# Performance work log

Measured on AMD Instinct MI355X. Metric: run time of the kernel, lower is better.

Reference implementation:

```python
import jax, jax.numpy as jnp
import numpy as np

DIM = 768
H = 12
HD = 64  # head_dim = dim // num_heads
SCALE = HD ** (-0.5)
EPS = 1e-6


def setup_inputs() -> dict:
    key = jax.random.key(0)
    k1, k2, k3, k4, k5 = jax.random.split(key, 5)
    B, N = 8, 1024
    x = jax.random.normal(k1, (B, N, DIM), dtype=jnp.float32)
    policy = jax.random.uniform(k2, (B, N, 1), dtype=jnp.float32)
    # nn.Linear weights: [out_features, in_features]; qkv_bias=False, proj has bias
    qkv_w = jax.random.normal(k3, (3 * H * HD, DIM), dtype=jnp.float32) * (DIM ** -0.5)
    proj_w = jax.random.normal(k4, (DIM, H * HD), dtype=jnp.float32) * ((H * HD) ** -0.5)
    proj_b = jax.random.normal(k5, (DIM,), dtype=jnp.float32) * 0.01
    return {"x": x, "policy": policy, "qkv_w": qkv_w, "proj_w": proj_w, "proj_b": proj_b}


def _softmax_with_policy(attn, policy):
    # attn: [B,H,N,N], policy: [B,N,1]
    B, Hh, N, _ = attn.shape
    attn_policy = policy.reshape(B, 1, 1, N)
    eye = jnp.eye(N, dtype=attn_policy.dtype).reshape(1, 1, N, N)
    attn_policy = attn_policy + (1.0 - attn_policy) * eye
    max_att = jnp.max(attn, axis=-1, keepdims=True)
    a = jnp.exp((attn - max_att).astype(jnp.float32)) * attn_policy.astype(jnp.float32)
    a = (a + EPS / N) / (jnp.sum(a, axis=-1, keepdims=True) + EPS)
    return a.astype(max_att.dtype)


def reference(x, policy, qkv_w, proj_w, proj_b):
    B, N, C = x.shape
    qkv = (x @ qkv_w.T).reshape(B, N, 3, H, HD)
    qkv = jnp.transpose(qkv, (2, 0, 3, 1, 4))  # [3,B,H,N,HD]
    q, k, v = qkv[0], qkv[1], qkv[2]
    attn = jnp.einsum('bhnd,bhmd->bhnm', q * SCALE, k)  # [B,H,N,N]
    attn = _softmax_with_policy(attn, policy)
    out = jnp.einsum('bhnm,bhmd->bhnd', attn, v)  # [B,H,N,HD]
    out = jnp.transpose(out, (0, 2, 1, 3)).reshape(B, N, H * HD)
    return out @ proj_w.T + proj_b
```

## Files before the change

### kernel.cpp

```cpp
#include <hip/hip_runtime.h>

typedef __bf16 bf16x8 __attribute__((ext_vector_type(8)));
typedef float floatx4 __attribute__((ext_vector_type(4)));

#define EPSF 1e-6f

__device__ inline unsigned short f2bf(float f) {
  union { float f; unsigned u; } x; x.f = f;
  unsigned r = x.u + 0x7FFFu + ((x.u >> 16) & 1u);
  return (unsigned short)(r >> 16);
}
__device__ inline float bf2f(unsigned short u) {
  union { unsigned u; float f; } x; x.u = ((unsigned)u) << 16;
  return x.f;
}
__device__ inline unsigned pk2bf(float lo, float hi) {
  union { float f; unsigned u; } a, b; a.f = lo; b.f = hi;
  unsigned ua = a.u + 0x8000u, ub = b.u + 0x8000u;
  return (ub & 0xFFFF0000u) | (ua >> 16);
}
__device__ inline float fexp2(float x) { return __builtin_amdgcn_exp2f(x); }

__device__ inline floatx4 mfma16(bf16x8 a, bf16x8 b, floatx4 c) {
  return __builtin_amdgcn_mfma_f32_16x16x32_bf16(a, b, c, 0, 0, 0);
}

__device__ inline void gll16(const unsigned short* g, unsigned short* l) {
  __builtin_amdgcn_global_load_lds((__attribute__((address_space(1))) void*)g,
                                   (__attribute__((address_space(3))) void*)l, 16, 0, 0);
}

__device__ __host__ inline int sigma_inv(int p) {
  const int qq = p >> 3, jj = p & 7;
  return (jj < 4) ? (qq * 4 + jj) : (16 + qq * 4 + jj - 4);
}

__global__ __launch_bounds__(256) void prep_kernel(const float* __restrict__ x,
                                                   const float* __restrict__ qkv_w,
                                                   const float* __restrict__ proj_w,
                                                   const float* __restrict__ policy,
                                                   unsigned short* __restrict__ xb,
                                                   unsigned short* __restrict__ wqkv,
                                                   unsigned short* __restrict__ wproj,
                                                   unsigned short* __restrict__ pbf) {
  const int bid = blockIdx.x, tid = threadIdx.x;
  if (bid < 3072) {
    const int i = bid * 2048 + tid * 8;
    float4 v0 = *(const float4*)(x + i);
    float4 v1 = *(const float4*)(x + i + 4);
    __align__(16) unsigned short o[8] = {f2bf(v0.x), f2bf(v0.y), f2bf(v0.z), f2bf(v0.w),
                                         f2bf(v1.x), f2bf(v1.y), f2bf(v1.z), f2bf(v1.w)};
    *(float4*)(xb + i) = *(float4*)o;
  } else if (bid < 3936) {
    const int i = (bid - 3072) * 2048 + tid * 8;
    const float s = (i < 589824) ? 0.18033688011112042f : 1.0f;
    float4 v0 = *(const float4*)(qkv_w + i);
    float4 v1 = *(const float4*)(qkv_w + i + 4);
    __align__(16) unsigned short o[8] = {
        f2bf(v0.x * s), f2bf(v0.y * s), f2bf(v0.z * s), f2bf(v0.w * s),
        f2bf(v1.x * s), f2bf(v1.y * s), f2bf(v1.z * s), f2bf(v1.w * s)};
    *(float4*)(wqkv + i) = *(float4*)o;
  } else if (bid < 4224) {
    const int i0 = (bid - 3936) * 2048 + tid * 8;
    const int base = (i0 / 768) * 768 + ((i0 % 768) & ~63);
    __align__(16) unsigned short o[8];
#pragma unroll
    for (int t = 0; t < 8; t++) {
      const int cp = (i0 + t) & 63;
      const int c = 16 * (cp & 3) + (cp >> 2);
      o[t] = f2bf(proj_w[base + c]);
    }
    *(float4*)(wproj + i0) = *(float4*)o;
  } else {
    const int idx = (bid - 4224) * 256 + tid;
    const int b = idx >> 10, g = idx & 1023;
    const int c = ((g >> 5) << 5) + sigma_inv(g & 31);
    pbf[idx] = f2bf(policy[b * 1024 + c]);
  }
}

template <int EP, int BN>
__global__ __launch_bounds__(256, 3) void gemm_bt(const unsigned short* __restrict__ A,
                                                  const unsigned short* __restrict__ Bt,
                                                  void* __restrict__ Cout,
                                                  const float* __restrict__ bias,
                                                  int M, int N, int K) {
  constexpr int J = BN / 32;
  __shared__ __align__(16) unsigned short sA[128 * 64];
  __shared__ __align__(16) unsigned short sB[BN * 64];
  const int m0 = blockIdx.y * 128, n0 = blockIdx.x * BN;
  const int tid = threadIdx.x;
  const int lane = tid & 63, wave = tid >> 6;
  const int qd = lane >> 4, l15 = lane & 15;
  const int wr = (wave >> 1) * 64, wc = (wave & 1) * (BN / 2);
  const int srow = tid >> 3;
  const int scb = (tid & 7) ^ (srow & 7);
  const unsigned short* Ag = A + (long)(m0 + srow) * K + scb * 8;
  const unsigned short* Bg = Bt + (long)(n0 + srow) * K + scb * 8;
  const int x7 = l15 & 7;
  floatx4 acc[4][J] = {};
  for (int k0 = 0; k0 < K; k0 += 64) {
    __syncthreads();
#pragma unroll
    for (int p = 0; p < 4; p++) gll16(Ag + (long)(p * 32) * K + k0, sA + p * 2048 + wave * 512);
#pragma unroll
    for (int p = 0; p < J; p++) gll16(Bg + (long)(p * 32) * K + k0, sB + p * 2048 + wave * 512);
    __syncthreads();
#pragma unroll
    for (int s = 0; s < 2; s++) {
      const int cw = ((s * 4 + qd) ^ x7) * 8;
      bf16x8 af[4], bf[J];
#pragma unroll
      for (int i = 0; i < 4; i++) af[i] = *(const bf16x8*)&sA[(wr + i * 16 + l15) * 64 + cw];
#pragma unroll
      for (int j = 0; j < J; j++) bf[j] = *(const bf16x8*)&sB[(wc + j * 16 + l15) * 64 + cw];
#pragma unroll
      for (int i = 0; i < 4; i++)
#pragma unroll
        for (int j = 0; j < J; j++) acc[i][j] = mfma16(af[i], bf[j], acc[i][j]);
    }
  }
  if constexpr (EP == 0) {
#pragma unroll
    for (int i = 0; i < 4; i++)
#pragma unroll
      for (int r = 0; r < 4; r++) {
        const int row = m0 + wr + i * 16 + qd * 4 + r;
        __align__(8) unsigned short pk[4];
#pragma unroll
        for (int j = 0; j < 4; j++) pk[j] = f2bf(acc[i][j][r]);
        *(uint2*)((unsigned short*)Cout + (long)row * N + n0 + wc + 4 * l15) = *(uint2*)pk;
      }
  } else {
#pragma unroll
    for (int i = 0; i < 4; i++)
#pragma unroll
      for (int j = 0; j < J; j++) {
        const int col = n0 + wc + j * 16 + l15;
#pragma unroll
        for (int r = 0; r < 4; r++) {
          const int row = m0 + wr + i * 16 + qd * 4 + r;
          ((float*)Cout)[(long)row * N + col] = acc[i][j][r] + bias[col];
        }
      }
  }
}

__global__ __launch_bounds__(256) void transpose_v(const unsigned short* __restrict__ qkv,
                                                   const float* __restrict__ policy,
                                                   unsigned short* __restrict__ vTp) {
  __shared__ unsigned short tile[64][72];
  __shared__ float sPol[64];
  const int bh = blockIdx.y;
  const int b = bh / 12, h = bh % 12;
  const int n0 = blockIdx.x * 64;
  const int t = threadIdx.x;
  if (t < 64) sPol[t] = policy[b * 1024 + n0 + t];
  {
    const int nr = t >> 2, dc = (t & 3) * 16;
    const unsigned short* src = qkv + (long)(b * 1024 + n0 + nr) * 2304 + 2 * 768 + h * 64 + dc;
    float4 v0 = *(const float4*)src;
    float4 v1 = *(const float4*)(src + 8);
    *(float4*)&tile[nr][dc] = v0;
    *(float4*)&tile[nr][dc + 8] = v1;
  }
  __syncthreads();
  {
    const int d = t >> 2, nc = (t & 3) * 16;
    __align__(16) unsigned short o[16];
#pragma unroll
    for (int jj = 0; jj < 16; jj++) {
      const int cc = nc + jj;
      const int cl = (cc & 32) + sigma_inv(cc & 31);
      o[jj] = f2bf(bf2f(tile[cl][d]) * sPol[cl]);
    }
    unsigned short* dst = vTp + (long)(bh * 64 + d) * 1024 + n0 + nc;
    *(float4*)dst = *(float4*)&o[0];
    *(float4*)(dst + 8) = *(float4*)&o[8];
  }
}

__global__ __launch_bounds__(256, 3) void attn_kernel(const unsigned short* __restrict__ qkv,
                                                      const unsigned short* __restrict__ vTp,
                                                      const unsigned short* __restrict__ pbf,
                                                      const float* __restrict__ policy,
                                                      unsigned short* __restrict__ aout) {
  __shared__ __align__(16) unsigned short sK[2][2048];
  __shared__ __align__(16) unsigned short sV[2][2048];
  __shared__ __align__(16) unsigned short sPv[1024];
  __shared__ float sD[4][32];
  const int bid = blockIdx.x;
  const int bh = bid % 96, qt = bid / 96;
  const int b = bh / 12, h = bh % 12;
  const int tid = threadIdx.x;
  const int wave = tid >> 6, lane = tid & 63;
  const int qd = lane >> 4, l15 = lane & 15;
  const int q0 = qt * 128 + wave * 32;
  const unsigned short* qb = qkv + (long)(b * 1024 + q0 + l15) * 2304 + h * 64 + qd * 8;
  bf16x8 qf00 = *(const bf16x8*)qb;
  bf16x8 qf01 = *(const bf16x8*)(qb + 32);
  bf16x8 qf10 = *(const bf16x8*)(qb + (long)16 * 2304);
  bf16x8 qf11 = *(const bf16x8*)(qb + (long)16 * 2304 + 32);
  if (tid < 128) *(float4*)(sPv + tid * 8) = *(const float4*)(pbf + b * 1024 + tid * 8);
  const int krow = wave * 8 + (lane >> 3);
  const int kcb = (lane & 7) ^ (lane >> 3);
  const unsigned short* kgl = qkv + (long)(b * 1024 + krow) * 2304 + 768 + h * 64 + kcb * 8;
  const int vrow = tid >> 2;
  const int vcb = (tid & 3) ^ ((vrow ^ (vrow >> 2)) & 3);
  const unsigned short* vgl = vTp + (long)(bh * 64 + vrow) * 1024 + vcb * 8;
  const int x7 = l15 & 7;
  const int vsw = (qd ^ ((l15 ^ (l15 >> 2)) & 3)) * 8;
  floatx4 O0[4] = {}, O1[4] = {};
  floatx4 Dl0 = {}, Dl1 = {};
  gll16(kgl, &sK[0][wave * 512]);
  gll16(vgl, &sV[0][wave * 512]);
  __builtin_amdgcn_s_waitcnt(0);
  __syncthreads();
  for (int it = 0; it < 32; ++it) {
    const int buf = it & 1;
    if (it < 31) {
      gll16(kgl + (long)(32 * (it + 1)) * 2304, &sK[buf ^ 1][wave * 512]);
      gll16(vgl + 32 * (it + 1), &sV[buf ^ 1][wave * 512]);
    }
    const int c0 = it * 32;
    bf16x8 k00 = *(const bf16x8*)&sK[buf][(0 * 16 + l15) * 64 + ((0 + qd) ^ x7) * 8];
    bf16x8 k01 = *(const bf16x8*)&sK[buf][(0 * 16 + l15) * 64 + ((4 + qd) ^ x7) * 8];
    bf16x8 k10 = *(const bf16x8*)&sK[buf][(1 * 16 + l15) * 64 + ((0 + qd) ^ x7) * 8];
    bf16x8 k11 = *(const bf16x8*)&sK[buf][(1 * 16 + l15) * 64 + ((4 + qd) ^ x7) * 8];
    bf16x8 pv = *(const bf16x8*)&sPv[c0 + qd * 8];
    floatx4 z = {0.f, 0.f, 0.f, 0.f};
    floatx4 tA0 = mfma16(k01, qf01, mfma16(k00, qf00, z));
    floatx4 tB0 = mfma16(k11, qf01, mfma16(k10, qf00, z));
    floatx4 tA1 = mfma16(k01, qf11, mfma16(k00, qf10, z));
    floatx4 tB1 = mfma16(k11, qf11, mfma16(k10, qf10, z));
    uint4 pu0, pu1;
    pu0.x = pk2bf(fexp2(tA0[0]), fexp2(tA0[1]));
    pu0.y = pk2bf(fexp2(tA0[2]), fexp2(tA0[3]));
    pu0.z = pk2bf(fexp2(tB0[0]), fexp2(tB0[1]));
    pu0.w = pk2bf(fexp2(tB0[2]), fexp2(tB0[3]));
    pu1.x = pk2bf(fexp2(tA1[0]), fexp2(tA1[1]));
    pu1.y = pk2bf(fexp2(tA1[2]), fexp2(tA1[3]));
    pu1.z = pk2bf(fexp2(tB1[0]), fexp2(tB1[1]));
    pu1.w = pk2bf(fexp2(tB1[2]), fexp2(tB1[3]));
    bf16x8 pf0 = *(bf16x8*)&pu0;
    bf16x8 pf1 = *(bf16x8*)&pu1;
    bf16x8 vf0 = *(const bf16x8*)&sV[buf][(0 * 16 + l15) * 32 + vsw];
    bf16x8 vf1 = *(const bf16x8*)&sV[buf][(1 * 16 + l15) * 32 + vsw];
    bf16x8 vf2 = *(const bf16x8*)&sV[buf][(2 * 16 + l15) * 32 + vsw];
    bf16x8 vf3 = *(const bf16x8*)&sV[buf][(3 * 16 + l15) * 32 + vsw];
    Dl0 = mfma16(pf0, pv, Dl0);
    Dl1 = mfma16(pf1, pv, Dl1);
    O0[0] = mfma16(pf0, vf0, O0[0]); O1[0] = mfma16(pf1, vf0, O1[0]);
    O0[1] = mfma16(pf0, vf1, O0[1]); O1[1] = mfma16(pf1, vf1, O1[1]);
    O0[2] = mfma16(pf0, vf2, O0[2]); O1[2] = mfma16(pf1, vf2, O1[2]);
    O0[3] = mfma16(pf0, vf3, O0[3]); O1[3] = mfma16(pf1, vf3, O1[3]);
    __builtin_amdgcn_s_waitcnt(0);
    __syncthreads();
  }
  {
    const unsigned short* kd = qkv + (long)(b * 1024 + q0 + l15) * 2304 + 768 + h * 64 + qd * 8;
    bf16x8 kd00 = *(const bf16x8*)kd;
    bf16x8 kd01 = *(const bf16x8*)(kd + 32);
    bf16x8 kd10 = *(const bf16x8*)(kd + (long)16 * 2304);
    bf16x8 kd11 = *(const bf16x8*)(kd + (long)16 * 2304 + 32);
    float part0 = 0.f, part1 = 0.f;
#pragma unroll
    for (int jj = 0; jj < 8; jj++) {
      part0 += (float)qf00[jj] * (float)kd00[jj] + (float)qf01[jj] * (float)kd01[jj];
      part1 += (float)qf10[jj] * (float)kd10[jj] + (float)qf11[jj] * (float)kd11[jj];
    }
    part0 += __shfl_xor(part0, 16); part0 += __shfl_xor(part0, 32);
    part1 += __shfl_xor(part1, 16); part1 += __shfl_xor(part1, 32);
    const float p0 = policy[b * 1024 + q0 + l15];
    const float p1 = policy[b * 1024 + q0 + 16 + l15];
    if (qd == 0) {
      sD[wave][l15] = fexp2(part0) * (1.0f - p0);
      sD[wave][16 + l15] = fexp2(part1) * (1.0f - p1);
    }
    __builtin_amdgcn_s_waitcnt(0);
    const unsigned short* vdiag = qkv + (long)(b * 1024 + q0) * 2304 + 1536 + h * 64 + l15;
#pragma unroll
    for (int r = 0; r < 4; r++) {
      const int row = qd * 4 + r;
      const float c0v = sD[wave][row], c1v = sD[wave][16 + row];
#pragma unroll
      for (int j = 0; j < 4; j++) {
        O0[j][r] += c0v * bf2f(vdiag[(long)row * 2304 + j * 16]);
        O1[j][r] += c1v * bf2f(vdiag[(long)(16 + row) * 2304 + j * 16]);
      }
      Dl0[r] += c0v;
      Dl1[r] += c1v;
    }
  }
  const long ob = (long)(b * 1024 + q0 + qd * 4) * 768 + h * 64 + l15;
#pragma unroll
  for (int r = 0; r < 4; r++) {
    const float li0 = 1.0f / (Dl0[r] + EPSF);
    const float li1 = 1.0f / (Dl1[r] + EPSF);
#pragma unroll
    for (int j = 0; j < 4; j++) {
      aout[ob + (long)r * 768 + j * 16] = f2bf(O0[j][r] * li0);
      aout[ob + (long)(16 * 768) + r * 768 + j * 16] = f2bf(O1[j][r] * li1);
    }
  }
}

extern "C" void kernel_launch(void* const* d_in, const int* in_sizes, int n_in,
                              void* d_out, int out_size, void* d_ws, size_t ws_size,
                              hipStream_t stream) {
  const float* x      = (const float*)d_in[0];
  const float* policy = (const float*)d_in[1];
  const float* qkv_w  = (const float*)d_in[2];
  const float* proj_w = (const float*)d_in[3];
  const float* proj_b = (const float*)d_in[4];
  float* out = (float*)d_out;

  char* ws = (char*)d_ws;
  unsigned short* xb    = (unsigned short*)(ws + 0);
  unsigned short* wqkv  = (unsigned short*)(ws + 12582912);
  unsigned short* wproj = (unsigned short*)(ws + 16121856);
  unsigned short* qkvb  = (unsigned short*)(ws + 17301504);
  unsigned short* vTp   = (unsigned short*)(ws + 55050240);
  unsigned short* aoutb = (unsigned short*)(ws + 67633152);
  unsigned short* pbf   = (unsigned short*)(ws + 80216064);

  prep_kernel<<<4256, 256, 0, stream>>>(x, qkv_w, proj_w, policy, xb, wqkv, wproj, pbf);
  gemm_bt<0, 128><<<dim3(18, 64), 256, 0, stream>>>(xb, wqkv, qkvb, nullptr, 8192, 2304, 768);
  transpose_v<<<dim3(16, 96), 256, 0, stream>>>(qkvb, policy, vTp);
  attn_kernel<<<dim3(768), 256, 0, stream>>>(qkvb, vTp, pbf, policy, aoutb);
  gemm_bt<1, 64><<<dim3(12, 64), 256, 0, stream>>>(aoutb, wproj, out, proj_b, 8192, 768, 768);
}
```

Baseline: 186.1 us.

## Double-buffer GEMM K-tiles and widen attention KV tile per iteration

```diff
diff --git a/kernel.cpp b/kernel.cpp
--- a/kernel.cpp
+++ b/kernel.cpp
@@ -86,39 +86,47 @@
                                                   const float* __restrict__ bias,
                                                   int M, int N, int K) {
   constexpr int J = BN / 32;
-  __shared__ __align__(16) unsigned short sA[128 * 64];
-  __shared__ __align__(16) unsigned short sB[BN * 64];
+  __shared__ __align__(16) unsigned short sA[2][128 * 32];
+  __shared__ __align__(16) unsigned short sB[2][BN * 32];
   const int m0 = blockIdx.y * 128, n0 = blockIdx.x * BN;
   const int tid = threadIdx.x;
   const int lane = tid & 63, wave = tid >> 6;
   const int qd = lane >> 4, l15 = lane & 15;
   const int wr = (wave >> 1) * 64, wc = (wave & 1) * (BN / 2);
-  const int srow = tid >> 3;
-  const int scb = (tid & 7) ^ (srow & 7);
+  const int srow = tid >> 2;
+  const int scb = (tid & 3) ^ (srow & 3);
   const unsigned short* Ag = A + (long)(m0 + srow) * K + scb * 8;
   const unsigned short* Bg = Bt + (long)(n0 + srow) * K + scb * 8;
-  const int x7 = l15 & 7;
+  const int x3 = l15 & 3;
+  const int nit = K / 32;
   floatx4 acc[4][J] = {};
-  for (int k0 = 0; k0 < K; k0 += 64) {
+  gll16(Ag, &sA[0][wave * 512]);
+  gll16(Ag + (long)64 * K, &sA[0][2048 + wave * 512]);
+  gll16(Bg, &sB[0][wave * 512]);
+  if (BN == 128) gll16(Bg + (long)64 * K, &sB[0][2048 + wave * 512]);
+  __builtin_amdgcn_s_waitcnt(0);
+  __syncthreads();
+  for (int it = 0; it < nit; ++it) {
+    const int buf = it & 1;
+    if (it + 1 < nit) {
+      const long k0 = 32 * (it + 1);
+      gll16(Ag + k0, &sA[buf ^ 1][wave * 512]);
+      gll16(Ag + (long)64 * K + k0, &sA[buf ^ 1][2048 + wave * 512]);
+      gll16(Bg + k0, &sB[buf ^ 1][wave * 512]);
+      if (BN == 128) gll16(Bg + (long)64 * K + k0, &sB[buf ^ 1][2048 + wave * 512]);
+    }
+    const int cw = (qd ^ x3) * 8;
+    bf16x8 af[4], bf[J];
+#pragma unroll
+    for (int i = 0; i < 4; i++) af[i] = *(const bf16x8*)&sA[buf][(wr + i * 16 + l15) * 32 + cw];
+#pragma unroll
+    for (int j = 0; j < J; j++) bf[j] = *(const bf16x8*)&sB[buf][(wc + j * 16 + l15) * 32 + cw];
+#pragma unroll
+    for (int i = 0; i < 4; i++)
+#pragma unroll
+      for (int j = 0; j < J; j++) acc[i][j] = mfma16(af[i], bf[j], acc[i][j]);
+    __builtin_amdgcn_s_waitcnt(0);
     __syncthreads();
-#pragma unroll
-    for (int p = 0; p < 4; p++) gll16(Ag + (long)(p * 32) * K + k0, sA + p * 2048 + wave * 512);
-#pragma unroll
-    for (int p = 0; p < J; p++) gll16(Bg + (long)(p * 32) * K + k0, sB + p * 2048 + wave * 512);
-    __syncthreads();
-#pragma unroll
-    for (int s = 0; s < 2; s++) {
-      const int cw = ((s * 4 + qd) ^ x7) * 8;
-      bf16x8 af[4], bf[J];
-#pragma unroll
-      for (int i = 0; i < 4; i++) af[i] = *(const bf16x8*)&sA[(wr + i * 16 + l15) * 64 + cw];
-#pragma unroll
-      for (int j = 0; j < J; j++) bf[j] = *(const bf16x8*)&sB[(wc + j * 16 + l15) * 64 + cw];
-#pragma unroll
-      for (int i = 0; i < 4; i++)
-#pragma unroll
-        for (int j = 0; j < J; j++) acc[i][j] = mfma16(af[i], bf[j], acc[i][j]);
-    }
   }
   if constexpr (EP == 0) {
 #pragma unroll
@@ -185,8 +193,8 @@
                                                       const unsigned short* __restrict__ pbf,
                                                       const float* __restrict__ policy,
                                                       unsigned short* __restrict__ aout) {
-  __shared__ __align__(16) unsigned short sK[2][2048];
-  __shared__ __align__(16) unsigned short sV[2][2048];
+  __shared__ __align__(16) unsigned short sK[2][4096];
+  __shared__ __align__(16) unsigned short sV[2][4096];
   __shared__ __align__(16) unsigned short sPv[1024];
   __shared__ float sD[4][32];
   const int bid = blockIdx.x;
@@ -213,47 +221,55 @@
   floatx4 O0[4] = {}, O1[4] = {};
   floatx4 Dl0 = {}, Dl1 = {};
   gll16(kgl, &sK[0][wave * 512]);
+  gll16(kgl + (long)32 * 2304, &sK[0][2048 + wave * 512]);
   gll16(vgl, &sV[0][wave * 512]);
+  gll16(vgl + 32, &sV[0][2048 + wave * 512]);
   __builtin_amdgcn_s_waitcnt(0);
   __syncthreads();
-  for (int it = 0; it < 32; ++it) {
+  for (int it = 0; it < 16; ++it) {
     const int buf = it & 1;
-    if (it < 31) {
-      gll16(kgl + (long)(32 * (it + 1)) * 2304, &sK[buf ^ 1][wave * 512]);
-      gll16(vgl + 32 * (it + 1), &sV[buf ^ 1][wave * 512]);
-    }
-    const int c0 = it * 32;
-    bf16x8 k00 = *(const bf16x8*)&sK[buf][(0 * 16 + l15) * 64 + ((0 + qd) ^ x7) * 8];
-    bf16x8 k01 = *(const bf16x8*)&sK[buf][(0 * 16 + l15) * 64 + ((4 + qd) ^ x7) * 8];
-    bf16x8 k10 = *(const bf16x8*)&sK[buf][(1 * 16 + l15) * 64 + ((0 + qd) ^ x7) * 8];
-    bf16x8 k11 = *(const bf16x8*)&sK[buf][(1 * 16 + l15) * 64 + ((4 + qd) ^ x7) * 8];
-    bf16x8 pv = *(const bf16x8*)&sPv[c0 + qd * 8];
-    floatx4 z = {0.f, 0.f, 0.f, 0.f};
-    floatx4 tA0 = mfma16(k01, qf01, mfma16(k00, qf00, z));
-    floatx4 tB0 = mfma16(k11, qf01, mfma16(k10, qf00, z));
-    floatx4 tA1 = mfma16(k01, qf11, mfma16(k00, qf10, z));
-    floatx4 tB1 = mfma16(k11, qf11, mfma16(k10, qf10, z));
-    uint4 pu0, pu1;
-    pu0.x = pk2bf(fexp2(tA0[0]), fexp2(tA0[1]));
-    pu0.y = pk2bf(fexp2(tA0[2]), fexp2(tA0[3]));
-    pu0.z = pk2bf(fexp2(tB0[0]), fexp2(tB0[1]));
-    pu0.w = pk2bf(fexp2(tB0[2]), fexp2(tB0[3]));
-    pu1.x = pk2bf(fexp2(tA1[0]), fexp2(tA1[1]));
-    pu1.y = pk2bf(fexp2(tA1[2]), fexp2(tA1[3]));
-    pu1.z = pk2bf(fexp2(tB1[0]), fexp2(tB1[1]));
-    pu1.w = pk2bf(fexp2(tB1[2]), fexp2(tB1[3]));
-    bf16x8 pf0 = *(bf16x8*)&pu0;
-    bf16x8 pf1 = *(bf16x8*)&pu1;
-    bf16x8 vf0 = *(const bf16x8*)&sV[buf][(0 * 16 + l15) * 32 + vsw];
-    bf16x8 vf1 = *(const bf16x8*)&sV[buf][(1 * 16 + l15) * 32 + vsw];
-    bf16x8 vf2 = *(const bf16x8*)&sV[buf][(2 * 16 + l15) * 32 + vsw];
-    bf16x8 vf3 = *(const bf16x8*)&sV[buf][(3 * 16 + l15) * 32 + vsw];
-    Dl0 = mfma16(pf0, pv, Dl0);
-    Dl1 = mfma16(pf1, pv, Dl1);
-    O0[0] = mfma16(pf0, vf0, O0[0]); O1[0] = mfma16(pf1, vf0, O1[0]);
-    O0[1] = mfma16(pf0, vf1, O0[1]); O1[1] = mfma16(pf1, vf1, O1[1]);
-    O0[2] = mfma16(pf0, vf2, O0[2]); O1[2] = mfma16(pf1, vf2, O1[2]);
-    O0[3] = mfma16(pf0, vf3, O0[3]); O1[3] = mfma16(pf1, vf3, O1[3]);
+    if (it < 15) {
+      const long cn = 64 * (it + 1);
+      gll16(kgl + cn * 2304, &sK[buf ^ 1][wave * 512]);
+      gll16(kgl + (cn + 32) * 2304, &sK[buf ^ 1][2048 + wave * 512]);
+      gll16(vgl + cn, &sV[buf ^ 1][wave * 512]);
+      gll16(vgl + cn + 32, &sV[buf ^ 1][2048 + wave * 512]);
+    }
+    const int c0 = it * 64;
+#pragma unroll
+    for (int g = 0; g < 2; g++) {
+      bf16x8 k00 = *(const bf16x8*)&sK[buf][((g * 2 + 0) * 16 + l15) * 64 + ((0 + qd) ^ x7) * 8];
+      bf16x8 k01 = *(const bf16x8*)&sK[buf][((g * 2 + 0) * 16 + l15) * 64 + ((4 + qd) ^ x7) * 8];
+      bf16x8 k10 = *(const bf16x8*)&sK[buf][((g * 2 + 1) * 16 + l15) * 64 + ((0 + qd) ^ x7) * 8];
+      bf16x8 k11 = *(const bf16x8*)&sK[buf][((g * 2 + 1) * 16 + l15) * 64 + ((4 + qd) ^ x7) * 8];
+      bf16x8 pv = *(const bf16x8*)&sPv[c0 + g * 32 + qd * 8];
+      floatx4 z = {0.f, 0.f, 0.f, 0.f};
+      floatx4 tA0 = mfma16(k01, qf01, mfma16(k00, qf00, z));
+      floatx4 tB0 = mfma16(k11, qf01, mfma16(k10, qf00, z));
+      floatx4 tA1 = mfma16(k01, qf11, mfma16(k00, qf10, z));
+      floatx4 tB1 = mfma16(k11, qf11, mfma16(k10, qf10, z));
+      uint4 pu0, pu1;
+      pu0.x = pk2bf(fexp2(tA0[0]), fexp2(tA0[1]));
+      pu0.y = pk2bf(fexp2(tA0[2]), fexp2(tA0[3]));
+      pu0.z = pk2bf(fexp2(tB0[0]), fexp2(tB0[1]));
+      pu0.w = pk2bf(fexp2(tB0[2]), fexp2(tB0[3]));
+      pu1.x = pk2bf(fexp2(tA1[0]), fexp2(tA1[1]));
+      pu1.y = pk2bf(fexp2(tA1[2]), fexp2(tA1[3]));
+      pu1.z = pk2bf(fexp2(tB1[0]), fexp2(tB1[1]));
+      pu1.w = pk2bf(fexp2(tB1[2]), fexp2(tB1[3]));
+      bf16x8 pf0 = *(bf16x8*)&pu0;
+      bf16x8 pf1 = *(bf16x8*)&pu1;
+      bf16x8 vf0 = *(const bf16x8*)&sV[buf][g * 2048 + (0 * 16 + l15) * 32 + vsw];
+      bf16x8 vf1 = *(const bf16x8*)&sV[buf][g * 2048 + (1 * 16 + l15) * 32 + vsw];
+      bf16x8 vf2 = *(const bf16x8*)&sV[buf][g * 2048 + (2 * 16 + l15) * 32 + vsw];
+      bf16x8 vf3 = *(const bf16x8*)&sV[buf][g * 2048 + (3 * 16 + l15) * 32 + vsw];
+      Dl0 = mfma16(pf0, pv, Dl0);
+      Dl1 = mfma16(pf1, pv, Dl1);
+      O0[0] = mfma16(pf0, vf0, O0[0]); O1[0] = mfma16(pf1, vf0, O1[0]);
+      O0[1] = mfma16(pf0, vf1, O0[1]); O1[1] = mfma16(pf1, vf1, O1[1]);
+      O0[2] = mfma16(pf0, vf2, O0[2]); O1[2] = mfma16(pf1, vf2, O1[2]);
+      O0[3] = mfma16(pf0, vf3, O0[3]); O1[3] = mfma16(pf1, vf3, O1[3]);
+    }
     __builtin_amdgcn_s_waitcnt(0);
     __syncthreads();
   }
```

New measurement: 197.8 us. +6.3%, slower.
